# Kernel optimization log

Hardware: AMD Instinct MI355X
Metric: run time of the kernel (lower is better)

Reference implementation:

```python
import jax, jax.numpy as jnp
import numpy as np

IN_FEATURES_LS = (32, 64, 128, 256)
OUT_FEATURES = 1024
B, T = 16, 4096


def setup_inputs() -> dict:
    key = jax.random.key(0)
    k_x, k_idx, k_w, k_b = jax.random.split(key, 4)
    n = len(IN_FEATURES_LS)
    x = jax.random.normal(k_x, (B, T, OUT_FEATURES), dtype=jnp.float32)
    # per-row declared feature size, drawn from the configured list
    branch_idx = jax.random.randint(k_idx, (B, T), 0, n)
    in_feat_size = jnp.array(IN_FEATURES_LS, dtype=jnp.int32)[branch_idx]
    # kaiming_uniform_(a=sqrt(5)) on (n, out, out): fan_in = out, bound = 1/sqrt(fan_in)
    bound_w = 1.0 / np.sqrt(OUT_FEATURES)
    weight = jax.random.uniform(k_w, (n, OUT_FEATURES, OUT_FEATURES), dtype=jnp.float32,
                                minval=-bound_w, maxval=bound_w)
    bound_b = 1.0 / np.sqrt(OUT_FEATURES)
    bias = jax.random.uniform(k_b, (n, OUT_FEATURES), dtype=jnp.float32,
                              minval=-bound_b, maxval=bound_b)
    return {"x": x, "in_feat_size": in_feat_size, "weight": weight, "bias": bias}


def reference(x, in_feat_size, weight, bias):
    # Loop over the small fixed set of feature-size branches (matches original).
    out = jnp.zeros(x.shape[:-1] + (OUT_FEATURES,), dtype=x.dtype)
    for idx, feat_size in enumerate(IN_FEATURES_LS):
        mask = (in_feat_size == feat_size)[..., None].astype(x.dtype)  # [B,T,1]
        y = jnp.einsum('oi,bti->bto', weight[idx], x) + bias[idx]
        out = out + mask * y
    return out
```

## Files before the change

### kernel.cpp

```cpp
#include <hip/hip_runtime.h>
#include <hip/hip_bf16.h>

#define OUTF 1024
#define NROWS 65536
#define NBR 4
#define XBROWS 66560
#define NWG 1040

typedef __attribute__((ext_vector_type(8))) short short8;
typedef __attribute__((ext_vector_type(4))) float f32x4;

__device__ inline unsigned short f2bf(float f) {
    return __builtin_bit_cast(unsigned short, (__bf16)f);
}
__device__ inline void gload_lds16(const void* g, void* l) {
    __builtin_amdgcn_global_load_lds(
        (const __attribute__((address_space(1))) void*)g,
        (__attribute__((address_space(3))) void*)l, 16, 0, 0);
}
__device__ inline short8 pack8(float4 a, float4 b) {
    short8 o;
    o[0] = (short)f2bf(a.x); o[1] = (short)f2bf(a.y);
    o[2] = (short)f2bf(a.z); o[3] = (short)f2bf(a.w);
    o[4] = (short)f2bf(b.x); o[5] = (short)f2bf(b.y);
    o[6] = (short)f2bf(b.z); o[7] = (short)f2bf(b.w);
    return o;
}

__global__ void k_count(const int* __restrict__ feat, int* __restrict__ cnt) {
    __shared__ int lc[NBR];
    int tid = threadIdx.x;
    if (tid < NBR) lc[tid] = 0;
    __syncthreads();
    int r = blockIdx.x * 256 + tid;
    int b = 26 - __clz(feat[r]);
    atomicAdd(&lc[b], 1);
    __syncthreads();
    if (tid < NBR && lc[tid]) atomicAdd(&cnt[tid], lc[tid]);
}

__global__ void k_prefix(int* __restrict__ ws) {
    if (threadIdx.x == 0) {
        int s = 0;
        for (int b = 0; b < NBR; b++) {
            ws[4 + b] = s;
            s = (s + ws[b] + 255) & ~255;
            ws[8 + b] = 0;
        }
    }
}

__global__ void k_fill(const int* __restrict__ feat, int* __restrict__ ws,
                       int* __restrict__ rowlist) {
    int tid = threadIdx.x;
    int lane = tid & 63;
    int r = blockIdx.x * 256 + tid;
    int b = 26 - __clz(feat[r]);
    #pragma unroll
    for (int bb = 0; bb < NBR; bb++) {
        unsigned long long mask = __ballot(b == bb);
        int leader = __ffsll((long long)mask) - 1;
        int cntw = __popcll(mask);
        int basepos = 0;
        if (lane == leader) basepos = atomicAdd(&ws[8 + bb], cntw);
        basepos = __shfl(basepos, leader < 0 ? 0 : leader);
        if (b == bb) {
            int prefix = __popcll(mask & ((1ull << lane) - 1ull));
            rowlist[ws[4 + bb] + basepos + prefix] = r;
        }
    }
}

__global__ void k_convw(const float* __restrict__ w, unsigned short* __restrict__ wsw) {
    int idx = (int)blockIdx.x * 256 + (int)threadIdx.x;
    int branch = idx >> 17;
    int rem = idx & 131071;
    int n = rem >> 7;
    int cb = (rem & 127) << 4;
    int kw = cb >> 7;
    int wb_ = cb & 127;
    int src = kw * 64 + ((wb_ ^ ((n & 7) << 4)) >> 1);
    const float4* s = reinterpret_cast<const float4*>(
        w + ((size_t)branch << 20) + (size_t)n * OUTF + src);
    char* dst = reinterpret_cast<char*>(wsw) + ((size_t)branch << 21) + (size_t)n * 2048 + cb;
    *reinterpret_cast<short8*>(dst) = pack8(s[0], s[1]);
}

__global__ void k_convx(const float* __restrict__ x, const int* __restrict__ rowlist,
                        unsigned short* __restrict__ xb) {
    int g = (int)blockIdx.x * 512 + (int)threadIdx.x;
    int orow = g >> 7;
    int cb = (g & 127) << 4;
    int rl = rowlist[orow];
    if ((unsigned)rl >= NROWS) rl = 0;
    int kw = cb >> 7;
    int wb_ = cb & 127;
    int src = kw * 64 + ((wb_ ^ ((orow & 7) << 4)) >> 1);
    const float4* s = reinterpret_cast<const float4*>(x + (size_t)rl * OUTF + src);
    char* dst = reinterpret_cast<char*>(xb) + (size_t)orow * 2048 + cb;
    *reinterpret_cast<short8*>(dst) = pack8(s[0], s[1]);
}

__global__ __launch_bounds__(512, 2)
void k_gemm5(const unsigned short* __restrict__ xb,
             const unsigned short* __restrict__ wsw,
             const float* __restrict__ bias,
             const int* __restrict__ ws_i,
             const int* __restrict__ rowlist,
             float* __restrict__ out) {
    extern __shared__ char lds[];

    const int d = (int)blockIdx.x;
    const int work = (d & 7) * (NWG >> 3) + (d >> 3);
    const int mtile = work >> 2;
    const int ntile = work & 3;

    int branch = -1, lt = 0, cnt = 0, rbase = 0;
    int t_ = mtile;
    #pragma unroll
    for (int b = 0; b < NBR; b++) {
        if (branch < 0) {
            int c = ws_i[b];
            int nt = (c + 255) >> 8;
            if (t_ < nt) { branch = b; lt = t_; cnt = c; rbase = ws_i[4 + b]; }
            else t_ -= nt;
        }
    }
    if (branch < 0) return;

    const int tid = threadIdx.x;
    const int lane = tid & 63;
    const int w8 = tid >> 6;
    const int wm = (w8 >> 2) * 128;
    const int wn = (w8 & 3) * 64;
    const int n0 = ntile * 256;
    const int row0 = rbase + lt * 256;

    const char* gA[4];
    const char* gB[4];
    #pragma unroll
    for (int i = 0; i < 4; i++) {
        int r = i * 64 + (tid >> 3);
        gA[i] = reinterpret_cast<const char*>(xb) + (size_t)(row0 + r) * 2048 + ((tid & 7) << 4);
        gB[i] = reinterpret_cast<const char*>(wsw) + ((size_t)branch << 21)
                + (size_t)(n0 + r) * 2048 + ((tid & 7) << 4);
    }
    const int ldsoff = tid << 4;

    f32x4 acc[8][4];
    #pragma unroll
    for (int i = 0; i < 8; i++)
        #pragma unroll
        for (int j = 0; j < 4; j++) acc[i][j] = (f32x4){0.f, 0.f, 0.f, 0.f};

    const int swz = (lane & 7) << 4;
    const int kq = (lane >> 4) << 4;
    const int arowb = (wm + (lane & 15)) * 128;
    const int browb = (wn + (lane & 15)) * 128;

    #pragma unroll
    for (int i = 0; i < 4; i++) gload_lds16(gA[i], lds + i * 8192 + ldsoff);
    #pragma unroll
    for (int i = 0; i < 4; i++) gload_lds16(gA[i] + 128, lds + 32768 + i * 8192 + ldsoff);
    #pragma unroll
    for (int i = 0; i < 4; i++) gload_lds16(gB[i], lds + 98304 + i * 8192 + ldsoff);
    asm volatile("s_waitcnt vmcnt(0)" ::: "memory");
    __builtin_amdgcn_sched_barrier(0);
    __builtin_amdgcn_s_barrier();
    __builtin_amdgcn_sched_barrier(0);

    int ia = 0;
    for (int t = 0; t < 16; ++t) {
        char* Ac = lds + ia * 32768;
        char* Bc = lds + 98304 + (t & 1) * 32768;

        if (t < 15) {
            char* Bn = lds + 98304 + ((t + 1) & 1) * 32768;
            #pragma unroll
            for (int i = 0; i < 4; i++)
                gload_lds16(gB[i] + (t + 1) * 128, Bn + i * 8192 + ldsoff);
        }
        if (t < 14) {
            int ia2 = ia + 2; if (ia2 >= 3) ia2 -= 3;
            char* An = lds + ia2 * 32768;
            #pragma unroll
            for (int i = 0; i < 4; i++)
                gload_lds16(gA[i] + (t + 2) * 128, An + i * 8192 + ldsoff);
        }
        __builtin_amdgcn_sched_barrier(0);

        __builtin_amdgcn_s_setprio(1);
        #pragma unroll
        for (int ks = 0; ks < 2; ks++) {
            const int kb = (ks << 6) + kq;
            short8 af[8], bf_[4];
            #pragma unroll
            for (int i = 0; i < 8; i++)
                af[i] = *reinterpret_cast<const short8*>(Ac + arowb + i * 2048 + (kb ^ swz));
            #pragma unroll
            for (int j = 0; j < 4; j++)
                bf_[j] = *reinterpret_cast<const short8*>(Bc + browb + j * 2048 + (kb ^ swz));
            #pragma unroll
            for (int i = 0; i < 8; i++)
                #pragma unroll
                for (int j = 0; j < 4; j++)
                    acc[i][j] = __builtin_amdgcn_mfma_f32_16x16x32_bf16(af[i], bf_[j], acc[i][j], 0, 0, 0);
        }
        __builtin_amdgcn_s_setprio(0);

        if (t < 14) { asm volatile("s_waitcnt vmcnt(4)" ::: "memory"); }
        else        { asm volatile("s_waitcnt vmcnt(0)" ::: "memory"); }
        __builtin_amdgcn_sched_barrier(0);
        __builtin_amdgcn_s_barrier();
        __builtin_amdgcn_sched_barrier(0);

        ia = (ia + 1 == 3) ? 0 : ia + 1;
    }

    const int ccol = lane & 15;
    const int crow = (lane >> 4) << 2;
    float bv[4];
    const float* bp = bias + branch * OUTF + n0 + wn;
    #pragma unroll
    for (int fn = 0; fn < 4; fn++) bv[fn] = bp[fn * 16 + ccol];
    #pragma unroll
    for (int fm = 0; fm < 8; fm++) {
        #pragma unroll
        for (int j = 0; j < 4; j++) {
            int gm = lt * 256 + wm + fm * 16 + crow + j;
            if (gm < cnt) {
                int orow = rowlist[rbase + gm];
                float* orp = out + (size_t)orow * OUTF + n0 + wn;
                #pragma unroll
                for (int fn = 0; fn < 4; fn++)
                    orp[fn * 16 + ccol] = acc[fm][fn][j] + bv[fn];
            }
        }
    }
}

__global__ __launch_bounds__(256, 3)
void k_gemm_fb(const float* __restrict__ x,
               const float* __restrict__ wf,
               const float* __restrict__ bias,
               const int* __restrict__ ws_i,
               const int* __restrict__ rowlist,
               float* __restrict__ out) {
    __shared__ unsigned short As[128][72];
    __shared__ unsigned short Bs[128][72];

    int t = (int)blockIdx.x;
    int branch = -1, ltile = 0, cnt = 0, rbase = 0;
    #pragma unroll
    for (int b = 0; b < NBR; b++) {
        if (branch < 0) {
            int c = ws_i[b];
            int nt = (c + 127) >> 7;
            if (t < nt) { branch = b; ltile = t; cnt = c; rbase = ws_i[4 + b]; }
            else t -= nt;
        }
    }
    if (branch < 0) return;

    const int tid = threadIdx.x;
    const int lane = tid & 63;
    const int wid = tid >> 6;
    const int wm = (wid & 1) << 6;
    const int wn = (wid >> 1) << 6;
    const int n0 = (int)blockIdx.y * 128;

    const int srow = tid >> 1;
    const int scol = (tid & 1) << 5;

    const int gmrow = ltile * 128 + srow;
    const int grow = (gmrow < cnt) ? rowlist[rbase + gmrow] : -1;
    const float* xsrc = x + (size_t)(grow < 0 ? 0 : grow) * OUTF + scol;
    const float* wfsrc = wf + ((size_t)branch << 20) + (size_t)(n0 + srow) * OUTF + scol;

    f32x4 acc[4][4];
    #pragma unroll
    for (int i = 0; i < 4; i++)
        #pragma unroll
        for (int j = 0; j < 4; j++)
            acc[i][j] = (f32x4){0.f, 0.f, 0.f, 0.f};

    for (int k0 = 0; k0 < OUTF; k0 += 64) {
        {
            unsigned short* dst = &As[srow][scol];
            if (grow >= 0) {
                const float4* s4 = reinterpret_cast<const float4*>(xsrc + k0);
                #pragma unroll
                for (int i = 0; i < 8; i += 2) {
                    float4 v0 = s4[i], v1 = s4[i + 1];
                    *reinterpret_cast<short8*>(dst + i * 4) = pack8(v0, v1);
                }
            } else {
                short8 z = (short8){0,0,0,0,0,0,0,0};
                #pragma unroll
                for (int i = 0; i < 8; i += 2) *reinterpret_cast<short8*>(dst + i * 4) = z;
            }
        }
        {
            unsigned short* dst = &Bs[srow][scol];
            const float4* s4 = reinterpret_cast<const float4*>(wfsrc + k0);
            #pragma unroll
            for (int i = 0; i < 8; i += 2) {
                float4 v0 = s4[i], v1 = s4[i + 1];
                *reinterpret_cast<short8*>(dst + i * 4) = pack8(v0, v1);
            }
        }
        __syncthreads();
        #pragma unroll
        for (int kk = 0; kk < 64; kk += 32) {
            const int krd = kk + (lane >> 4) * 8;
            short8 af[4], bf_[4];
            #pragma unroll
            for (int i = 0; i < 4; i++)
                af[i] = *reinterpret_cast<const short8*>(&As[wm + i * 16 + (lane & 15)][krd]);
            #pragma unroll
            for (int i = 0; i < 4; i++)
                bf_[i] = *reinterpret_cast<const short8*>(&Bs[wn + i * 16 + (lane & 15)][krd]);
            #pragma unroll
            for (int i = 0; i < 4; i++)
                #pragma unroll
                for (int j = 0; j < 4; j++)
                    acc[i][j] = __builtin_amdgcn_mfma_f32_16x16x32_bf16(af[i], bf_[j], acc[i][j], 0, 0, 0);
        }
        __syncthreads();
    }

    const int ccol = lane & 15;
    const int crow = (lane >> 4) << 2;
    float bv[4];
    const float* bp = bias + branch * OUTF + n0 + wn;
    #pragma unroll
    for (int fn = 0; fn < 4; fn++) bv[fn] = bp[fn * 16 + ccol];
    #pragma unroll
    for (int fm = 0; fm < 4; fm++) {
        #pragma unroll
        for (int j = 0; j < 4; j++) {
            int gm = ltile * 128 + wm + fm * 16 + crow + j;
            if (gm < cnt) {
                int orow = rowlist[rbase + gm];
                float* orp = out + (size_t)orow * OUTF + n0 + wn;
                #pragma unroll
                for (int fn = 0; fn < 4; fn++)
                    orp[fn * 16 + ccol] = acc[fm][fn][j] + bv[fn];
            }
        }
    }
}

extern "C" void kernel_launch(void* const* d_in, const int* in_sizes, int n_in,
                              void* d_out, int out_size, void* d_ws, size_t ws_size,
                              hipStream_t stream) {
    const float* x = (const float*)d_in[0];
    const int* feat = (const int*)d_in[1];
    const float* w = (const float*)d_in[2];
    const float* bias = (const float*)d_in[3];
    float* out = (float*)d_out;

    char* ws = (char*)d_ws;
    int* ws_i = (int*)ws;
    int* rowlist = (int*)(ws + 256);
    const size_t WSW_OFF = (size_t)512 << 10;
    const size_t XB_OFF = (size_t)9 << 20;
    unsigned short* wsw = (unsigned short*)(ws + WSW_OFF);
    unsigned short* xb = (unsigned short*)(ws + XB_OFF);
    const size_t need_full = XB_OFF + (size_t)XBROWS * 2048;

    (void)hipMemsetAsync(ws_i, 0, 64, stream);
    k_count<<<NROWS / 256, 256, 0, stream>>>(feat, ws_i);
    k_prefix<<<1, 64, 0, stream>>>(ws_i);
    k_fill<<<NROWS / 256, 256, 0, stream>>>(feat, ws_i, rowlist);

    if (ws_size >= need_full) {
        k_convw<<<2048, 256, 0, stream>>>(w, wsw);
        k_convx<<<(XBROWS * 128) / 512, 512, 0, stream>>>(x, rowlist, xb);
        (void)hipFuncSetAttribute((const void*)k_gemm5,
                                  hipFuncAttributeMaxDynamicSharedMemorySize, 163840);
        k_gemm5<<<NWG, 512, 163840, stream>>>(xb, wsw, bias, ws_i, rowlist, out);
    } else {
        dim3 grid(NROWS / 128 + NBR, OUTF / 128);
        k_gemm_fb<<<grid, 256, 0, stream>>>(x, w, bias, ws_i, rowlist, out);
    }
}
```

Before: 352.3 us.

## Restructure GEMM pipeline into 9-slot half-tile ring with finer barriers

The main GEMM now streams A and B in 64-wide K half-tiles through a 9-slot LDS ring, with loads issued between four MFMA sub-phases per iteration. This replaces the previous XOR-swizzled 128-wide K tiles that used triple and double buffers. The bf16 conversion kernels drop the swizzle and write a plain layout, and the fallback grid tiling is also adjusted. The aim is better overlap of global-to-LDS loads with MFMA work and less LDS use (147456 vs 163840 bytes). The cost is more barriers per K step, and LDS bank conflicts are possible without the swizzle.

```diff
diff --git a/kernel.cpp b/kernel.cpp
--- a/kernel.cpp
+++ b/kernel.cpp
@@ -26,6 +26,9 @@
     o[6] = (short)f2bf(b.z); o[7] = (short)f2bf(b.w);
     return o;
 }
+
+#define VMCNT(n) asm volatile("s_waitcnt vmcnt(" #n ")" ::: "memory")
+#define SBAR() do { __builtin_amdgcn_s_barrier(); __builtin_amdgcn_sched_barrier(0); } while (0)
 
 __global__ void k_count(const int* __restrict__ feat, int* __restrict__ cnt) {
     __shared__ int lc[NBR];
@@ -71,19 +74,10 @@
     }
 }
 
-__global__ void k_convw(const float* __restrict__ w, unsigned short* __restrict__ wsw) {
-    int idx = (int)blockIdx.x * 256 + (int)threadIdx.x;
-    int branch = idx >> 17;
-    int rem = idx & 131071;
-    int n = rem >> 7;
-    int cb = (rem & 127) << 4;
-    int kw = cb >> 7;
-    int wb_ = cb & 127;
-    int src = kw * 64 + ((wb_ ^ ((n & 7) << 4)) >> 1);
-    const float4* s = reinterpret_cast<const float4*>(
-        w + ((size_t)branch << 20) + (size_t)n * OUTF + src);
-    char* dst = reinterpret_cast<char*>(wsw) + ((size_t)branch << 21) + (size_t)n * 2048 + cb;
-    *reinterpret_cast<short8*>(dst) = pack8(s[0], s[1]);
+__global__ void k_convw(const float* __restrict__ w, unsigned short* __restrict__ wb) {
+    int i = ((int)blockIdx.x * 256 + (int)threadIdx.x) * 8;
+    const float4* s = reinterpret_cast<const float4*>(w + i);
+    *reinterpret_cast<short8*>(wb + i) = pack8(s[0], s[1]);
 }
 
 __global__ void k_convx(const float* __restrict__ x, const int* __restrict__ rowlist,
@@ -93,17 +87,14 @@
     int cb = (g & 127) << 4;
     int rl = rowlist[orow];
     if ((unsigned)rl >= NROWS) rl = 0;
-    int kw = cb >> 7;
-    int wb_ = cb & 127;
-    int src = kw * 64 + ((wb_ ^ ((orow & 7) << 4)) >> 1);
-    const float4* s = reinterpret_cast<const float4*>(x + (size_t)rl * OUTF + src);
-    char* dst = reinterpret_cast<char*>(xb) + (size_t)orow * 2048 + cb;
-    *reinterpret_cast<short8*>(dst) = pack8(s[0], s[1]);
+    const float4* s = reinterpret_cast<const float4*>(x + (size_t)rl * OUTF + (cb >> 1));
+    *reinterpret_cast<short8*>(reinterpret_cast<char*>(xb) + (size_t)orow * 2048 + cb) =
+        pack8(s[0], s[1]);
 }
 
 __global__ __launch_bounds__(512, 2)
-void k_gemm5(const unsigned short* __restrict__ xb,
-             const unsigned short* __restrict__ wsw,
+void k_gemm6(const unsigned short* __restrict__ xb,
+             const unsigned short* __restrict__ wb,
              const float* __restrict__ bias,
              const int* __restrict__ ws_i,
              const int* __restrict__ rowlist,
@@ -136,16 +127,14 @@
     const int n0 = ntile * 256;
     const int row0 = rbase + lt * 256;
 
-    const char* gA[4];
-    const char* gB[4];
-    #pragma unroll
-    for (int i = 0; i < 4; i++) {
-        int r = i * 64 + (tid >> 3);
-        gA[i] = reinterpret_cast<const char*>(xb) + (size_t)(row0 + r) * 2048 + ((tid & 7) << 4);
-        gB[i] = reinterpret_cast<const char*>(wsw) + ((size_t)branch << 21)
-                + (size_t)(n0 + r) * 2048 + ((tid & 7) << 4);
-    }
-    const int ldsoff = tid << 4;
+    const char* aSrc = reinterpret_cast<const char*>(xb)
+                       + (size_t)(row0 + (tid >> 2)) * 2048 + ((tid & 3) << 4);
+    const char* bSrc = reinterpret_cast<const char*>(wb) + ((size_t)branch << 21)
+                       + (size_t)(n0 + (tid >> 2)) * 2048 + ((tid & 3) << 4);
+    const int ldst = tid << 4;
+
+    const int aoff = (wm + (lane & 15)) * 64 + ((lane >> 4) << 4);
+    const int boff = (wn + (lane & 15)) * 64 + ((lane >> 4) << 4);
 
     f32x4 acc[8][4];
     #pragma unroll
@@ -153,69 +142,85 @@
         #pragma unroll
         for (int j = 0; j < 4; j++) acc[i][j] = (f32x4){0.f, 0.f, 0.f, 0.f};
 
-    const int swz = (lane & 7) << 4;
-    const int kq = (lane >> 4) << 4;
-    const int arowb = (wm + (lane & 15)) * 128;
-    const int browb = (wn + (lane & 15)) * 128;
-
-    #pragma unroll
-    for (int i = 0; i < 4; i++) gload_lds16(gA[i], lds + i * 8192 + ldsoff);
-    #pragma unroll
-    for (int i = 0; i < 4; i++) gload_lds16(gA[i] + 128, lds + 32768 + i * 8192 + ldsoff);
-    #pragma unroll
-    for (int i = 0; i < 4; i++) gload_lds16(gB[i], lds + 98304 + i * 8192 + ldsoff);
-    asm volatile("s_waitcnt vmcnt(0)" ::: "memory");
-    __builtin_amdgcn_sched_barrier(0);
-    __builtin_amdgcn_s_barrier();
-    __builtin_amdgcn_sched_barrier(0);
-
-    int ia = 0;
+    #define STAGE(u) do {                                                  \
+        const int _sl = (u) % 9;                                           \
+        const char* _s = ((u) & 1) ? bSrc : aSrc;                          \
+        const int _kb = (((u) >> 2) << 7) + ((((u) >> 1) & 1) << 6);       \
+        char* _d = lds + _sl * 16384 + ldst;                               \
+        gload_lds16(_s + _kb, _d);                                         \
+        gload_lds16(_s + 262144 + _kb, _d + 8192);                         \
+    } while (0)
+
+    STAGE(0); STAGE(1); STAGE(2); STAGE(3); STAGE(4); STAGE(5);
+    VMCNT(8);
+    SBAR();
+
+    short8 af[8], b0, b1;
+
     for (int t = 0; t < 16; ++t) {
-        char* Ac = lds + ia * 32768;
-        char* Bc = lds + 98304 + (t & 1) * 32768;
-
-        if (t < 15) {
-            char* Bn = lds + 98304 + ((t + 1) & 1) * 32768;
-            #pragma unroll
-            for (int i = 0; i < 4; i++)
-                gload_lds16(gB[i] + (t + 1) * 128, Bn + i * 8192 + ldsoff);
-        }
-        if (t < 14) {
-            int ia2 = ia + 2; if (ia2 >= 3) ia2 -= 3;
-            char* An = lds + ia2 * 32768;
-            #pragma unroll
-            for (int i = 0; i < 4; i++)
-                gload_lds16(gA[i] + (t + 2) * 128, An + i * 8192 + ldsoff);
-        }
-        __builtin_amdgcn_sched_barrier(0);
-
+        const int b4 = 4 * t;
+        char* A0 = lds + (b4 % 9) * 16384;
+        char* B0 = lds + ((b4 + 1) % 9) * 16384;
+        char* A1 = lds + ((b4 + 2) % 9) * 16384;
+        char* B1 = lds + ((b4 + 3) % 9) * 16384;
+
+        if (t < 15) STAGE(b4 + 6);
+        #pragma unroll
+        for (int i = 0; i < 8; i++)
+            af[i] = *reinterpret_cast<const short8*>(A0 + aoff + i * 1024);
+        b0 = *reinterpret_cast<const short8*>(B0 + boff);
+        b1 = *reinterpret_cast<const short8*>(B0 + boff + 1024);
         __builtin_amdgcn_s_setprio(1);
         #pragma unroll
-        for (int ks = 0; ks < 2; ks++) {
-            const int kb = (ks << 6) + kq;
-            short8 af[8], bf_[4];
-            #pragma unroll
-            for (int i = 0; i < 8; i++)
-                af[i] = *reinterpret_cast<const short8*>(Ac + arowb + i * 2048 + (kb ^ swz));
-            #pragma unroll
-            for (int j = 0; j < 4; j++)
-                bf_[j] = *reinterpret_cast<const short8*>(Bc + browb + j * 2048 + (kb ^ swz));
-            #pragma unroll
-            for (int i = 0; i < 8; i++)
-                #pragma unroll
-                for (int j = 0; j < 4; j++)
-                    acc[i][j] = __builtin_amdgcn_mfma_f32_16x16x32_bf16(af[i], bf_[j], acc[i][j], 0, 0, 0);
+        for (int i = 0; i < 8; i++) {
+            acc[i][0] = __builtin_amdgcn_mfma_f32_16x16x32_bf16(af[i], b0, acc[i][0], 0, 0, 0);
+            acc[i][1] = __builtin_amdgcn_mfma_f32_16x16x32_bf16(af[i], b1, acc[i][1], 0, 0, 0);
         }
         __builtin_amdgcn_s_setprio(0);
-
-        if (t < 14) { asm volatile("s_waitcnt vmcnt(4)" ::: "memory"); }
-        else        { asm volatile("s_waitcnt vmcnt(0)" ::: "memory"); }
-        __builtin_amdgcn_sched_barrier(0);
-        __builtin_amdgcn_s_barrier();
-        __builtin_amdgcn_sched_barrier(0);
-
-        ia = (ia + 1 == 3) ? 0 : ia + 1;
-    }
+        SBAR();
+
+        if (t < 15) STAGE(b4 + 7);
+        b0 = *reinterpret_cast<const short8*>(B0 + boff + 2048);
+        b1 = *reinterpret_cast<const short8*>(B0 + boff + 3072);
+        __builtin_amdgcn_s_setprio(1);
+        #pragma unroll
+        for (int i = 0; i < 8; i++) {
+            acc[i][2] = __builtin_amdgcn_mfma_f32_16x16x32_bf16(af[i], b0, acc[i][2], 0, 0, 0);
+            acc[i][3] = __builtin_amdgcn_mfma_f32_16x16x32_bf16(af[i], b1, acc[i][3], 0, 0, 0);
+        }
+        __builtin_amdgcn_s_setprio(0);
+        if (t < 15) { VMCNT(8); } else { VMCNT(0); }
+        SBAR();
+
+        if (t < 14) STAGE(b4 + 8);
+        #pragma unroll
+        for (int i = 0; i < 8; i++)
+            af[i] = *reinterpret_cast<const short8*>(A1 + aoff + i * 1024);
+        b0 = *reinterpret_cast<const short8*>(B1 + boff);
+        b1 = *reinterpret_cast<const short8*>(B1 + boff + 1024);
+        __builtin_amdgcn_s_setprio(1);
+        #pragma unroll
+        for (int i = 0; i < 8; i++) {
+            acc[i][0] = __builtin_amdgcn_mfma_f32_16x16x32_bf16(af[i], b0, acc[i][0], 0, 0, 0);
+            acc[i][1] = __builtin_amdgcn_mfma_f32_16x16x32_bf16(af[i], b1, acc[i][1], 0, 0, 0);
+        }
+        __builtin_amdgcn_s_setprio(0);
+        SBAR();
+
+        if (t < 14) STAGE(b4 + 9);
+        b0 = *reinterpret_cast<const short8*>(B1 + boff + 2048);
+        b1 = *reinterpret_cast<const short8*>(B1 + boff + 3072);
+        __builtin_amdgcn_s_setprio(1);
+        #pragma unroll
+        for (int i = 0; i < 8; i++) {
+            acc[i][2] = __builtin_amdgcn_mfma_f32_16x16x32_bf16(af[i], b0, acc[i][2], 0, 0, 0);
+            acc[i][3] = __builtin_amdgcn_mfma_f32_16x16x32_bf16(af[i], b1, acc[i][3], 0, 0, 0);
+        }
+        __builtin_amdgcn_s_setprio(0);
+        if (t < 14) { VMCNT(8); } else if (t == 14) { VMCNT(4); }
+        SBAR();
+    }
+    #undef STAGE
 
     const int ccol = lane & 15;
     const int crow = (lane >> 4) << 2;
@@ -255,7 +260,8 @@
     for (int b = 0; b < NBR; b++) {
         if (branch < 0) {
             int c = ws_i[b];
-            int nt = (c + 127) >> 7;
+            int nt = (c + 255) >> 8;
+            nt <<= 1;
             if (t < nt) { branch = b; ltile = t; cnt = c; rbase = ws_i[4 + b]; }
             else t -= nt;
         }
@@ -290,12 +296,10 @@
             if (grow >= 0) {
                 const float4* s4 = reinterpret_cast<const float4*>(xsrc + k0);
                 #pragma unroll
-                for (int i = 0; i < 8; i += 2) {
-                    float4 v0 = s4[i], v1 = s4[i + 1];
-                    *reinterpret_cast<short8*>(dst + i * 4) = pack8(v0, v1);
-                }
+                for (int i = 0; i < 8; i += 2)
+                    *reinterpret_cast<short8*>(dst + i * 4) = pack8(s4[i], s4[i + 1]);
             } else {
-                short8 z = (short8){0,0,0,0,0,0,0,0};
+                short8 z = (short8){0, 0, 0, 0, 0, 0, 0, 0};
                 #pragma unroll
                 for (int i = 0; i < 8; i += 2) *reinterpret_cast<short8*>(dst + i * 4) = z;
             }
@@ -304,10 +308,8 @@
             unsigned short* dst = &Bs[srow][scol];
             const float4* s4 = reinterpret_cast<const float4*>(wfsrc + k0);
             #pragma unroll
-            for (int i = 0; i < 8; i += 2) {
-                float4 v0 = s4[i], v1 = s4[i + 1];
-                *reinterpret_cast<short8*>(dst + i * 4) = pack8(v0, v1);
-            }
+            for (int i = 0; i < 8; i += 2)
+                *reinterpret_cast<short8*>(dst + i * 4) = pack8(s4[i], s4[i + 1]);
         }
         __syncthreads();
         #pragma unroll
@@ -363,9 +365,9 @@
     char* ws = (char*)d_ws;
     int* ws_i = (int*)ws;
     int* rowlist = (int*)(ws + 256);
-    const size_t WSW_OFF = (size_t)512 << 10;
+    const size_t WB_OFF = (size_t)512 << 10;
     const size_t XB_OFF = (size_t)9 << 20;
-    unsigned short* wsw = (unsigned short*)(ws + WSW_OFF);
+    unsigned short* wb = (unsigned short*)(ws + WB_OFF);
     unsigned short* xb = (unsigned short*)(ws + XB_OFF);
     const size_t need_full = XB_OFF + (size_t)XBROWS * 2048;
 
@@ -375,13 +377,13 @@
     k_fill<<<NROWS / 256, 256, 0, stream>>>(feat, ws_i, rowlist);
 
     if (ws_size >= need_full) {
-        k_convw<<<2048, 256, 0, stream>>>(w, wsw);
+        k_convw<<<(NBR * OUTF * OUTF) / (256 * 8), 256, 0, stream>>>(w, wb);
         k_convx<<<(XBROWS * 128) / 512, 512, 0, stream>>>(x, rowlist, xb);
-        (void)hipFuncSetAttribute((const void*)k_gemm5,
-                                  hipFuncAttributeMaxDynamicSharedMemorySize, 163840);
-        k_gemm5<<<NWG, 512, 163840, stream>>>(xb, wsw, bias, ws_i, rowlist, out);
+        (void)hipFuncSetAttribute((const void*)k_gemm6,
+                                  hipFuncAttributeMaxDynamicSharedMemorySize, 147456);
+        k_gemm6<<<NWG, 512, 147456, stream>>>(xb, wb, bias, ws_i, rowlist, out);
     } else {
-        dim3 grid(NROWS / 128 + NBR, OUTF / 128);
+        dim3 grid(NROWS / 128 + 2 * NBR, OUTF / 128);
         k_gemm_fb<<<grid, 256, 0, stream>>>(x, w, bias, ws_i, rowlist, out);
     }
 }
```

Measured after the change: 364.5 us. 3.4% more time.

## Fuse x gather and bf16 conversion into GEMM, shrink tiles to 128x128

Applied to the files above, without the earlier changes.

Removes the separate k_convx pass that gathered rows of x by branch into a bf16 swizzled buffer. The GEMM now loads fp32 x rows straight into LDS through the rowlist and converts them to bf16 in registers before the MFMA. Tiles shrink from 256x256 with 512 threads and a 3/2-stage pipeline to 128x128 with 256 threads. The new loop is single-buffered with two syncthreads per k-step. This saves a write and re-read of the bf16 copy of x, but it reads fp32 x from DRAM once per N-tile (8 times instead of 4) and gives up the prefetch overlap.

```diff
diff --git a/kernel.cpp b/kernel.cpp
--- a/kernel.cpp
+++ b/kernel.cpp
@@ -5,7 +5,7 @@
 #define NROWS 65536
 #define NBR 4
 #define XBROWS 66560
-#define NWG 1040
+#define NWG 4160
 
 typedef __attribute__((ext_vector_type(8))) short short8;
 typedef __attribute__((ext_vector_type(4))) float f32x4;
@@ -24,6 +24,14 @@
     o[2] = (short)f2bf(a.z); o[3] = (short)f2bf(a.w);
     o[4] = (short)f2bf(b.x); o[5] = (short)f2bf(b.y);
     o[6] = (short)f2bf(b.z); o[7] = (short)f2bf(b.w);
+    return o;
+}
+__device__ inline short8 pack8v(f32x4 a, f32x4 b) {
+    short8 o;
+    o[0] = (short)f2bf(a[0]); o[1] = (short)f2bf(a[1]);
+    o[2] = (short)f2bf(a[2]); o[3] = (short)f2bf(a[3]);
+    o[4] = (short)f2bf(b[0]); o[5] = (short)f2bf(b[1]);
+    o[6] = (short)f2bf(b[2]); o[7] = (short)f2bf(b[3]);
     return o;
 }
 
@@ -86,34 +94,20 @@
     *reinterpret_cast<short8*>(dst) = pack8(s[0], s[1]);
 }
 
-__global__ void k_convx(const float* __restrict__ x, const int* __restrict__ rowlist,
-                        unsigned short* __restrict__ xb) {
-    int g = (int)blockIdx.x * 512 + (int)threadIdx.x;
-    int orow = g >> 7;
-    int cb = (g & 127) << 4;
-    int rl = rowlist[orow];
-    if ((unsigned)rl >= NROWS) rl = 0;
-    int kw = cb >> 7;
-    int wb_ = cb & 127;
-    int src = kw * 64 + ((wb_ ^ ((orow & 7) << 4)) >> 1);
-    const float4* s = reinterpret_cast<const float4*>(x + (size_t)rl * OUTF + src);
-    char* dst = reinterpret_cast<char*>(xb) + (size_t)orow * 2048 + cb;
-    *reinterpret_cast<short8*>(dst) = pack8(s[0], s[1]);
-}
-
-__global__ __launch_bounds__(512, 2)
-void k_gemm5(const unsigned short* __restrict__ xb,
+__global__ __launch_bounds__(256, 3)
+void k_gemm7(const float* __restrict__ x,
              const unsigned short* __restrict__ wsw,
              const float* __restrict__ bias,
              const int* __restrict__ ws_i,
              const int* __restrict__ rowlist,
              float* __restrict__ out) {
-    extern __shared__ char lds[];
+    __shared__ char Alds[32768];
+    __shared__ char Blds[16384];
 
     const int d = (int)blockIdx.x;
     const int work = (d & 7) * (NWG >> 3) + (d >> 3);
-    const int mtile = work >> 2;
-    const int ntile = work & 3;
+    const int mtile = work >> 3;
+    const int ntile = work & 7;
 
     int branch = -1, lt = 0, cnt = 0, rbase = 0;
     int t_ = mtile;
@@ -121,100 +115,85 @@
     for (int b = 0; b < NBR; b++) {
         if (branch < 0) {
             int c = ws_i[b];
-            int nt = (c + 255) >> 8;
+            int nt = (c + 127) >> 7;
             if (t_ < nt) { branch = b; lt = t_; cnt = c; rbase = ws_i[4 + b]; }
             else t_ -= nt;
         }
     }
     if (branch < 0) return;
 
-    const int tid = threadIdx.x;
+    const int tid = (int)threadIdx.x;
     const int lane = tid & 63;
-    const int w8 = tid >> 6;
-    const int wm = (w8 >> 2) * 128;
-    const int wn = (w8 & 3) * 64;
-    const int n0 = ntile * 256;
-    const int row0 = rbase + lt * 256;
-
-    const char* gA[4];
-    const char* gB[4];
+    const int wid = tid >> 6;
+    const int wm = (wid & 1) << 6;
+    const int wn = (wid >> 1) << 6;
+    const int n0 = ntile << 7;
+    const int row0 = rbase + (lt << 7);
+
+    const char* aP[8];
+    {
+        const int rsub = tid >> 4;
+        const int sc = ((tid & 15) << 4) ^ ((rsub & 7) << 4);
+        #pragma unroll
+        for (int i = 0; i < 8; i++) {
+            int rl = rowlist[row0 + i * 16 + rsub];
+            if ((unsigned)rl >= NROWS) rl = 0;
+            aP[i] = reinterpret_cast<const char*>(x + (size_t)rl * OUTF) + sc;
+        }
+    }
+    const char* bP[4];
     #pragma unroll
     for (int i = 0; i < 4; i++) {
-        int r = i * 64 + (tid >> 3);
-        gA[i] = reinterpret_cast<const char*>(xb) + (size_t)(row0 + r) * 2048 + ((tid & 7) << 4);
-        gB[i] = reinterpret_cast<const char*>(wsw) + ((size_t)branch << 21)
-                + (size_t)(n0 + r) * 2048 + ((tid & 7) << 4);
-    }
-    const int ldsoff = tid << 4;
-
-    f32x4 acc[8][4];
-    #pragma unroll
-    for (int i = 0; i < 8; i++)
+        int rn = i * 32 + (tid >> 3);
+        bP[i] = reinterpret_cast<const char*>(wsw) + ((size_t)branch << 21)
+                + (size_t)(n0 + rn) * 2048 + ((tid & 7) << 4);
+    }
+    const int dst16 = tid << 4;
+
+    f32x4 acc[4][4];
+    #pragma unroll
+    for (int i = 0; i < 4; i++)
         #pragma unroll
         for (int j = 0; j < 4; j++) acc[i][j] = (f32x4){0.f, 0.f, 0.f, 0.f};
 
-    const int swz = (lane & 7) << 4;
-    const int kq = (lane >> 4) << 4;
-    const int arowb = (wm + (lane & 15)) * 128;
-    const int browb = (wn + (lane & 15)) * 128;
-
-    #pragma unroll
-    for (int i = 0; i < 4; i++) gload_lds16(gA[i], lds + i * 8192 + ldsoff);
-    #pragma unroll
-    for (int i = 0; i < 4; i++) gload_lds16(gA[i] + 128, lds + 32768 + i * 8192 + ldsoff);
-    #pragma unroll
-    for (int i = 0; i < 4; i++) gload_lds16(gB[i], lds + 98304 + i * 8192 + ldsoff);
-    asm volatile("s_waitcnt vmcnt(0)" ::: "memory");
-    __builtin_amdgcn_sched_barrier(0);
-    __builtin_amdgcn_s_barrier();
-    __builtin_amdgcn_sched_barrier(0);
-
-    int ia = 0;
-    for (int t = 0; t < 16; ++t) {
-        char* Ac = lds + ia * 32768;
-        char* Bc = lds + 98304 + (t & 1) * 32768;
-
-        if (t < 15) {
-            char* Bn = lds + 98304 + ((t + 1) & 1) * 32768;
+    const int q = lane >> 4;
+    const int lr = lane & 15;
+
+    for (int kt = 0; kt < 16; ++kt) {
+        #pragma unroll
+        for (int i = 0; i < 8; i++)
+            gload_lds16(aP[i] + kt * 256, Alds + i * 4096 + dst16);
+        #pragma unroll
+        for (int i = 0; i < 4; i++)
+            gload_lds16(bP[i] + kt * 128, Blds + i * 4096 + dst16);
+        __syncthreads();
+
+        #pragma unroll
+        for (int ks = 0; ks < 2; ks++) {
+            short8 af[4], bfr[4];
+            #pragma unroll
+            for (int i = 0; i < 4; i++) {
+                const int r = wm + i * 16 + lr;
+                const int off = ((ks << 7) + (q << 5)) ^ ((r & 7) << 4);
+                const f32x4 v0 = *reinterpret_cast<const f32x4*>(Alds + r * 256 + off);
+                const f32x4 v1 = *reinterpret_cast<const f32x4*>(Alds + r * 256 + (off ^ 16));
+                af[i] = pack8v(v0, v1);
+            }
+            #pragma unroll
+            for (int j = 0; j < 4; j++) {
+                const int r = wn + j * 16 + lr;
+                const int off = ((ks << 6) + (q << 4)) ^ ((r & 7) << 4);
+                bfr[j] = *reinterpret_cast<const short8*>(Blds + r * 128 + off);
+            }
+            __builtin_amdgcn_s_setprio(1);
             #pragma unroll
             for (int i = 0; i < 4; i++)
-                gload_lds16(gB[i] + (t + 1) * 128, Bn + i * 8192 + ldsoff);
-        }
-        if (t < 14) {
-            int ia2 = ia + 2; if (ia2 >= 3) ia2 -= 3;
-            char* An = lds + ia2 * 32768;
-            #pragma unroll
-            for (int i = 0; i < 4; i++)
-                gload_lds16(gA[i] + (t + 2) * 128, An + i * 8192 + ldsoff);
-        }
-        __builtin_amdgcn_sched_barrier(0);
-
-        __builtin_amdgcn_s_setprio(1);
-        #pragma unroll
-        for (int ks = 0; ks < 2; ks++) {
-            const int kb = (ks << 6) + kq;
-            short8 af[8], bf_[4];
-            #pragma unroll
-            for (int i = 0; i < 8; i++)
-                af[i] = *reinterpret_cast<const short8*>(Ac + arowb + i * 2048 + (kb ^ swz));
-            #pragma unroll
-            for (int j = 0; j < 4; j++)
-                bf_[j] = *reinterpret_cast<const short8*>(Bc + browb + j * 2048 + (kb ^ swz));
-            #pragma unroll
-            for (int i = 0; i < 8; i++)
                 #pragma unroll
                 for (int j = 0; j < 4; j++)
-                    acc[i][j] = __builtin_amdgcn_mfma_f32_16x16x32_bf16(af[i], bf_[j], acc[i][j], 0, 0, 0);
-        }
-        __builtin_amdgcn_s_setprio(0);
-
-        if (t < 14) { asm volatile("s_waitcnt vmcnt(4)" ::: "memory"); }
-        else        { asm volatile("s_waitcnt vmcnt(0)" ::: "memory"); }
-        __builtin_amdgcn_sched_barrier(0);
-        __builtin_amdgcn_s_barrier();
-        __builtin_amdgcn_sched_barrier(0);
-
-        ia = (ia + 1 == 3) ? 0 : ia + 1;
+                    acc[i][j] = __builtin_amdgcn_mfma_f32_16x16x32_bf16(af[i], bfr[j], acc[i][j], 0, 0, 0);
+            __builtin_amdgcn_s_setprio(0);
+        }
+        __syncthreads();
     }
 
     const int ccol = lane & 15;
@@ -224,10 +203,10 @@
     #pragma unroll
     for (int fn = 0; fn < 4; fn++) bv[fn] = bp[fn * 16 + ccol];
     #pragma unroll
-    for (int fm = 0; fm < 8; fm++) {
+    for (int fm = 0; fm < 4; fm++) {
         #pragma unroll
         for (int j = 0; j < 4; j++) {
-            int gm = lt * 256 + wm + fm * 16 + crow + j;
+            int gm = (lt << 7) + wm + fm * 16 + crow + j;
             if (gm < cnt) {
                 int orow = rowlist[rbase + gm];
                 float* orp = out + (size_t)orow * OUTF + n0 + wn;
@@ -290,12 +269,10 @@
             if (grow >= 0) {
                 const float4* s4 = reinterpret_cast<const float4*>(xsrc + k0);
                 #pragma unroll
-                for (int i = 0; i < 8; i += 2) {
-                    float4 v0 = s4[i], v1 = s4[i + 1];
-                    *reinterpret_cast<short8*>(dst + i * 4) = pack8(v0, v1);
-                }
+                for (int i = 0; i < 8; i += 2)
+                    *reinterpret_cast<short8*>(dst + i * 4) = pack8(s4[i], s4[i + 1]);
             } else {
-                short8 z = (short8){0,0,0,0,0,0,0,0};
+                short8 z = (short8){0, 0, 0, 0, 0, 0, 0, 0};
                 #pragma unroll
                 for (int i = 0; i < 8; i += 2) *reinterpret_cast<short8*>(dst + i * 4) = z;
             }
@@ -304,10 +281,8 @@
             unsigned short* dst = &Bs[srow][scol];
             const float4* s4 = reinterpret_cast<const float4*>(wfsrc + k0);
             #pragma unroll
-            for (int i = 0; i < 8; i += 2) {
-                float4 v0 = s4[i], v1 = s4[i + 1];
-                *reinterpret_cast<short8*>(dst + i * 4) = pack8(v0, v1);
-            }
+            for (int i = 0; i < 8; i += 2)
+                *reinterpret_cast<short8*>(dst + i * 4) = pack8(s4[i], s4[i + 1]);
         }
         __syncthreads();
         #pragma unroll
@@ -364,22 +339,17 @@
     int* ws_i = (int*)ws;
     int* rowlist = (int*)(ws + 256);
     const size_t WSW_OFF = (size_t)512 << 10;
-    const size_t XB_OFF = (size_t)9 << 20;
     unsigned short* wsw = (unsigned short*)(ws + WSW_OFF);
-    unsigned short* xb = (unsigned short*)(ws + XB_OFF);
-    const size_t need_full = XB_OFF + (size_t)XBROWS * 2048;
+    const size_t need = WSW_OFF + (size_t)NBR * OUTF * OUTF * 2;
 
     (void)hipMemsetAsync(ws_i, 0, 64, stream);
     k_count<<<NROWS / 256, 256, 0, stream>>>(feat, ws_i);
     k_prefix<<<1, 64, 0, stream>>>(ws_i);
     k_fill<<<NROWS / 256, 256, 0, stream>>>(feat, ws_i, rowlist);
 
-    if (ws_size >= need_full) {
+    if (ws_size >= need) {
         k_convw<<<2048, 256, 0, stream>>>(w, wsw);
-        k_convx<<<(XBROWS * 128) / 512, 512, 0, stream>>>(x, rowlist, xb);
-        (void)hipFuncSetAttribute((const void*)k_gemm5,
-                                  hipFuncAttributeMaxDynamicSharedMemorySize, 163840);
-        k_gemm5<<<NWG, 512, 163840, stream>>>(xb, wsw, bias, ws_i, rowlist, out);
+        k_gemm7<<<NWG, 256, 0, stream>>>(x, wsw, bias, ws_i, rowlist, out);
     } else {
         dim3 grid(NROWS / 128 + NBR, OUTF / 128);
         k_gemm_fb<<<grid, 256, 0, stream>>>(x, w, bias, ws_i, rowlist, out);
```

New measurement: 338.7 us. -3.9%, faster.

## Fuse x gather and bf16 conversion into GEMM, drop prefix kernel

Applied to the files above, without the earlier changes.

Removes the separate k_convx pass that gathered x rows into a bf16 staging buffer. The GEMM now loads fp32 rows through the rowlist into registers, converts them, and writes them into swizzled LDS, double-buffered one k-step ahead. The k_prefix kernel is replaced by recomputing segment bases inline. This saves a full write and re-read of the staged x and one launch, but the GEMM re-reads each x row in fp32 from all four n-tiles, and it now waits on vmcnt(0) every iteration, with shallower A prefetch than the old triple buffer.

```diff
diff --git a/kernel.cpp b/kernel.cpp
--- a/kernel.cpp
+++ b/kernel.cpp
@@ -25,6 +25,11 @@
     o[4] = (short)f2bf(b.x); o[5] = (short)f2bf(b.y);
     o[6] = (short)f2bf(b.z); o[7] = (short)f2bf(b.w);
     return o;
+}
+__device__ inline void seg_bases(const int* __restrict__ ws_i, int* base) {
+    int s = 0;
+    #pragma unroll
+    for (int b = 0; b < NBR; b++) { base[b] = s; s = (s + ws_i[b] + 255) & ~255; }
 }
 
 __global__ void k_count(const int* __restrict__ feat, int* __restrict__ cnt) {
@@ -39,19 +44,10 @@
     if (tid < NBR && lc[tid]) atomicAdd(&cnt[tid], lc[tid]);
 }
 
-__global__ void k_prefix(int* __restrict__ ws) {
-    if (threadIdx.x == 0) {
-        int s = 0;
-        for (int b = 0; b < NBR; b++) {
-            ws[4 + b] = s;
-            s = (s + ws[b] + 255) & ~255;
-            ws[8 + b] = 0;
-        }
-    }
-}
-
 __global__ void k_fill(const int* __restrict__ feat, int* __restrict__ ws,
                        int* __restrict__ rowlist) {
+    int base[NBR];
+    seg_bases(ws, base);
     int tid = threadIdx.x;
     int lane = tid & 63;
     int r = blockIdx.x * 256 + tid;
@@ -66,7 +62,7 @@
         basepos = __shfl(basepos, leader < 0 ? 0 : leader);
         if (b == bb) {
             int prefix = __popcll(mask & ((1ull << lane) - 1ull));
-            rowlist[ws[4 + bb] + basepos + prefix] = r;
+            rowlist[base[bb] + basepos + prefix] = r;
         }
     }
 }
@@ -86,23 +82,8 @@
     *reinterpret_cast<short8*>(dst) = pack8(s[0], s[1]);
 }
 
-__global__ void k_convx(const float* __restrict__ x, const int* __restrict__ rowlist,
-                        unsigned short* __restrict__ xb) {
-    int g = (int)blockIdx.x * 512 + (int)threadIdx.x;
-    int orow = g >> 7;
-    int cb = (g & 127) << 4;
-    int rl = rowlist[orow];
-    if ((unsigned)rl >= NROWS) rl = 0;
-    int kw = cb >> 7;
-    int wb_ = cb & 127;
-    int src = kw * 64 + ((wb_ ^ ((orow & 7) << 4)) >> 1);
-    const float4* s = reinterpret_cast<const float4*>(x + (size_t)rl * OUTF + src);
-    char* dst = reinterpret_cast<char*>(xb) + (size_t)orow * 2048 + cb;
-    *reinterpret_cast<short8*>(dst) = pack8(s[0], s[1]);
-}
-
 __global__ __launch_bounds__(512, 2)
-void k_gemm5(const unsigned short* __restrict__ xb,
+void k_gemm8(const float* __restrict__ x,
              const unsigned short* __restrict__ wsw,
              const float* __restrict__ bias,
              const int* __restrict__ ws_i,
@@ -115,6 +96,8 @@
     const int mtile = work >> 2;
     const int ntile = work & 3;
 
+    int bases[NBR];
+    seg_bases(ws_i, bases);
     int branch = -1, lt = 0, cnt = 0, rbase = 0;
     int t_ = mtile;
     #pragma unroll
@@ -122,13 +105,13 @@
         if (branch < 0) {
             int c = ws_i[b];
             int nt = (c + 255) >> 8;
-            if (t_ < nt) { branch = b; lt = t_; cnt = c; rbase = ws_i[4 + b]; }
+            if (t_ < nt) { branch = b; lt = t_; cnt = c; rbase = bases[b]; }
             else t_ -= nt;
         }
     }
     if (branch < 0) return;
 
-    const int tid = threadIdx.x;
+    const int tid = (int)threadIdx.x;
     const int lane = tid & 63;
     const int w8 = tid >> 6;
     const int wm = (w8 >> 2) * 128;
@@ -136,16 +119,25 @@
     const int n0 = ntile * 256;
     const int row0 = rbase + lt * 256;
 
-    const char* gA[4];
-    const char* gB[4];
+    const int sarow = tid >> 1;
+    const int h = tid & 1;
+    int arl = rowlist[row0 + sarow];
+    if ((unsigned)arl >= NROWS) arl = 0;
+    const float* aSrc = x + (size_t)arl * OUTF + h * 32;
+    const int arb = sarow * 128;
+    int awoff[4];
+    #pragma unroll
+    for (int j = 0; j < 4; j++)
+        awoff[j] = arb + (((h * 4 + j) << 4) ^ ((sarow & 7) << 4));
+
+    const char* gb[4];
     #pragma unroll
     for (int i = 0; i < 4; i++) {
-        int r = i * 64 + (tid >> 3);
-        gA[i] = reinterpret_cast<const char*>(xb) + (size_t)(row0 + r) * 2048 + ((tid & 7) << 4);
-        gB[i] = reinterpret_cast<const char*>(wsw) + ((size_t)branch << 21)
-                + (size_t)(n0 + r) * 2048 + ((tid & 7) << 4);
-    }
-    const int ldsoff = tid << 4;
+        int rn_ = i * 64 + (tid >> 3);
+        gb[i] = reinterpret_cast<const char*>(wsw) + ((size_t)branch << 21)
+                + (size_t)(n0 + rn_) * 2048 + ((tid & 7) << 4);
+    }
+    const int ldsoffB = tid << 4;
 
     f32x4 acc[8][4];
     #pragma unroll
@@ -158,63 +150,71 @@
     const int arowb = (wm + (lane & 15)) * 128;
     const int browb = (wn + (lane & 15)) * 128;
 
-    #pragma unroll
-    for (int i = 0; i < 4; i++) gload_lds16(gA[i], lds + i * 8192 + ldsoff);
-    #pragma unroll
-    for (int i = 0; i < 4; i++) gload_lds16(gA[i] + 128, lds + 32768 + i * 8192 + ldsoff);
-    #pragma unroll
-    for (int i = 0; i < 4; i++) gload_lds16(gB[i], lds + 98304 + i * 8192 + ldsoff);
-    asm volatile("s_waitcnt vmcnt(0)" ::: "memory");
-    __builtin_amdgcn_sched_barrier(0);
-    __builtin_amdgcn_s_barrier();
-    __builtin_amdgcn_sched_barrier(0);
-
-    int ia = 0;
+    {
+        #pragma unroll
+        for (int i = 0; i < 4; i++)
+            gload_lds16(gb[i], lds + 65536 + i * 8192 + ldsoffB);
+        const float4* p = reinterpret_cast<const float4*>(aSrc);
+        float4 r0 = p[0], r1 = p[1], r2 = p[2], r3 = p[3];
+        float4 r4 = p[4], r5 = p[5], r6 = p[6], r7 = p[7];
+        asm volatile("s_waitcnt vmcnt(0)" ::: "memory");
+        *reinterpret_cast<short8*>(lds + awoff[0]) = pack8(r0, r1);
+        *reinterpret_cast<short8*>(lds + awoff[1]) = pack8(r2, r3);
+        *reinterpret_cast<short8*>(lds + awoff[2]) = pack8(r4, r5);
+        *reinterpret_cast<short8*>(lds + awoff[3]) = pack8(r6, r7);
+        __syncthreads();
+    }
+
     for (int t = 0; t < 16; ++t) {
-        char* Ac = lds + ia * 32768;
-        char* Bc = lds + 98304 + (t & 1) * 32768;
+        char* Ac = lds + (t & 1) * 32768;
+        char* Bc = lds + 65536 + (t & 1) * 32768;
+        float4 rn[8];
 
         if (t < 15) {
-            char* Bn = lds + 98304 + ((t + 1) & 1) * 32768;
+            char* Bn = lds + 65536 + ((t + 1) & 1) * 32768;
             #pragma unroll
             for (int i = 0; i < 4; i++)
-                gload_lds16(gB[i] + (t + 1) * 128, Bn + i * 8192 + ldsoff);
-        }
-        if (t < 14) {
-            int ia2 = ia + 2; if (ia2 >= 3) ia2 -= 3;
-            char* An = lds + ia2 * 32768;
-            #pragma unroll
-            for (int i = 0; i < 4; i++)
-                gload_lds16(gA[i] + (t + 2) * 128, An + i * 8192 + ldsoff);
+                gload_lds16(gb[i] + (t + 1) * 128, Bn + i * 8192 + ldsoffB);
+            const float4* p = reinterpret_cast<const float4*>(aSrc + (t + 1) * 64);
+            #pragma unroll
+            for (int j = 0; j < 8; j++) rn[j] = p[j];
         }
         __builtin_amdgcn_sched_barrier(0);
 
-        __builtin_amdgcn_s_setprio(1);
         #pragma unroll
         for (int ks = 0; ks < 2; ks++) {
             const int kb = (ks << 6) + kq;
-            short8 af[8], bf_[4];
-            #pragma unroll
-            for (int i = 0; i < 8; i++)
-                af[i] = *reinterpret_cast<const short8*>(Ac + arowb + i * 2048 + (kb ^ swz));
+            short8 bf_[4];
             #pragma unroll
             for (int j = 0; j < 4; j++)
                 bf_[j] = *reinterpret_cast<const short8*>(Bc + browb + j * 2048 + (kb ^ swz));
             #pragma unroll
-            for (int i = 0; i < 8; i++)
-                #pragma unroll
-                for (int j = 0; j < 4; j++)
-                    acc[i][j] = __builtin_amdgcn_mfma_f32_16x16x32_bf16(af[i], bf_[j], acc[i][j], 0, 0, 0);
-        }
-        __builtin_amdgcn_s_setprio(0);
-
-        if (t < 14) { asm volatile("s_waitcnt vmcnt(4)" ::: "memory"); }
-        else        { asm volatile("s_waitcnt vmcnt(0)" ::: "memory"); }
-        __builtin_amdgcn_sched_barrier(0);
-        __builtin_amdgcn_s_barrier();
-        __builtin_amdgcn_sched_barrier(0);
-
-        ia = (ia + 1 == 3) ? 0 : ia + 1;
+            for (int hh = 0; hh < 2; hh++) {
+                short8 af[4];
+                #pragma unroll
+                for (int i = 0; i < 4; i++)
+                    af[i] = *reinterpret_cast<const short8*>(
+                        Ac + arowb + (hh * 4 + i) * 2048 + (kb ^ swz));
+                __builtin_amdgcn_s_setprio(1);
+                #pragma unroll
+                for (int i = 0; i < 4; i++)
+                    #pragma unroll
+                    for (int j = 0; j < 4; j++)
+                        acc[hh * 4 + i][j] = __builtin_amdgcn_mfma_f32_16x16x32_bf16(
+                            af[i], bf_[j], acc[hh * 4 + i][j], 0, 0, 0);
+                __builtin_amdgcn_s_setprio(0);
+            }
+        }
+
+        if (t < 15) {
+            asm volatile("s_waitcnt vmcnt(0)" ::: "memory");
+            char* An = lds + ((t + 1) & 1) * 32768;
+            *reinterpret_cast<short8*>(An + awoff[0]) = pack8(rn[0], rn[1]);
+            *reinterpret_cast<short8*>(An + awoff[1]) = pack8(rn[2], rn[3]);
+            *reinterpret_cast<short8*>(An + awoff[2]) = pack8(rn[4], rn[5]);
+            *reinterpret_cast<short8*>(An + awoff[3]) = pack8(rn[6], rn[7]);
+        }
+        __syncthreads();
     }
 
     const int ccol = lane & 15;
@@ -249,6 +249,8 @@
     __shared__ unsigned short As[128][72];
     __shared__ unsigned short Bs[128][72];
 
+    int bases[NBR];
+    seg_bases(ws_i, bases);
     int t = (int)blockIdx.x;
     int branch = -1, ltile = 0, cnt = 0, rbase = 0;
     #pragma unroll
@@ -256,7 +258,7 @@
         if (branch < 0) {
             int c = ws_i[b];
             int nt = (c + 127) >> 7;
-            if (t < nt) { branch = b; ltile = t; cnt = c; rbase = ws_i[4 + b]; }
+            if (t < nt) { branch = b; ltile = t; cnt = c; rbase = bases[b]; }
             else t -= nt;
         }
     }
@@ -273,8 +275,9 @@
     const int scol = (tid & 1) << 5;
 
     const int gmrow = ltile * 128 + srow;
-    const int grow = (gmrow < cnt) ? rowlist[rbase + gmrow] : -1;
-    const float* xsrc = x + (size_t)(grow < 0 ? 0 : grow) * OUTF + scol;
+    int grl = (gmrow < cnt) ? rowlist[rbase + gmrow] : -1;
+    if (grl >= NROWS) grl = -1;
+    const float* xsrc = x + (size_t)(grl < 0 ? 0 : grl) * OUTF + scol;
     const float* wfsrc = wf + ((size_t)branch << 20) + (size_t)(n0 + srow) * OUTF + scol;
 
     f32x4 acc[4][4];
@@ -287,15 +290,13 @@
     for (int k0 = 0; k0 < OUTF; k0 += 64) {
         {
             unsigned short* dst = &As[srow][scol];
-            if (grow >= 0) {
+            if (grl >= 0) {
                 const float4* s4 = reinterpret_cast<const float4*>(xsrc + k0);
                 #pragma unroll
-                for (int i = 0; i < 8; i += 2) {
-                    float4 v0 = s4[i], v1 = s4[i + 1];
-                    *reinterpret_cast<short8*>(dst + i * 4) = pack8(v0, v1);
-                }
+                for (int i = 0; i < 8; i += 2)
+                    *reinterpret_cast<short8*>(dst + i * 4) = pack8(s4[i], s4[i + 1]);
             } else {
-                short8 z = (short8){0,0,0,0,0,0,0,0};
+                short8 z = (short8){0, 0, 0, 0, 0, 0, 0, 0};
                 #pragma unroll
                 for (int i = 0; i < 8; i += 2) *reinterpret_cast<short8*>(dst + i * 4) = z;
             }
@@ -304,10 +305,8 @@
             unsigned short* dst = &Bs[srow][scol];
             const float4* s4 = reinterpret_cast<const float4*>(wfsrc + k0);
             #pragma unroll
-            for (int i = 0; i < 8; i += 2) {
-                float4 v0 = s4[i], v1 = s4[i + 1];
-                *reinterpret_cast<short8*>(dst + i * 4) = pack8(v0, v1);
-            }
+            for (int i = 0; i < 8; i += 2)
+                *reinterpret_cast<short8*>(dst + i * 4) = pack8(s4[i], s4[i + 1]);
         }
         __syncthreads();
         #pragma unroll
@@ -364,22 +363,18 @@
     int* ws_i = (int*)ws;
     int* rowlist = (int*)(ws + 256);
     const size_t WSW_OFF = (size_t)512 << 10;
-    const size_t XB_OFF = (size_t)9 << 20;
     unsigned short* wsw = (unsigned short*)(ws + WSW_OFF);
-    unsigned short* xb = (unsigned short*)(ws + XB_OFF);
-    const size_t need_full = XB_OFF + (size_t)XBROWS * 2048;
+    const size_t need = WSW_OFF + (size_t)NBR * OUTF * OUTF * 2;
 
     (void)hipMemsetAsync(ws_i, 0, 64, stream);
     k_count<<<NROWS / 256, 256, 0, stream>>>(feat, ws_i);
-    k_prefix<<<1, 64, 0, stream>>>(ws_i);
     k_fill<<<NROWS / 256, 256, 0, stream>>>(feat, ws_i, rowlist);
 
-    if (ws_size >= need_full) {
+    if (ws_size >= need) {
         k_convw<<<2048, 256, 0, stream>>>(w, wsw);
-        k_convx<<<(XBROWS * 128) / 512, 512, 0, stream>>>(x, rowlist, xb);
-        (void)hipFuncSetAttribute((const void*)k_gemm5,
-                                  hipFuncAttributeMaxDynamicSharedMemorySize, 163840);
-        k_gemm5<<<NWG, 512, 163840, stream>>>(xb, wsw, bias, ws_i, rowlist, out);
+        (void)hipFuncSetAttribute((const void*)k_gemm8,
+                                  hipFuncAttributeMaxDynamicSharedMemorySize, 131072);
+        k_gemm8<<<NWG, 512, 131072, stream>>>(x, wsw, bias, ws_i, rowlist, out);
     } else {
         dim3 grid(NROWS / 128 + NBR, OUTF / 128);
         k_gemm_fb<<<grid, 256, 0, stream>>>(x, w, bias, ws_i, rowlist, out);
```

Measured after the change: 438.3 us. +24.4%, slower.
